# Kernel tuning notes

Hardware: AMD Instinct MI355X
Metric: run time of the kernel (lower is better)

The kernel has to match this reference:

```python
import jax, jax.numpy as jnp
import numpy as np

N, E, G = 100000, 1600000, 256
F_IN, HID, NCLS = 16, 64, 2
EPS = 1e-5


def segment_mean(v, seg, num_segments):
    s = jax.ops.segment_sum(v, seg, num_segments=num_segments)
    c = jax.ops.segment_sum(jnp.ones((v.shape[0], 1), v.dtype), seg, num_segments=num_segments)
    return s / jnp.maximum(c, 1.0)


def graph_norm(x, seg, weight, bias, mean_scale):
    # PyG GraphNorm: per-graph mean/var with learnable mean_scale
    mean = segment_mean(x, seg, G)                      # [G, C]
    centered = x - mean_scale * mean[seg]               # [N, C]
    var = segment_mean(centered * centered, seg, G)     # [G, C]
    return weight * centered * jax.lax.rsqrt(var[seg] + EPS) + bias


def gcn_conv(x, W, b, row, col, n):
    # PyG GCNConv: h = x @ W; symmetric norm with added self-loops; scatter-add; + bias
    h = x @ W                                           # [N, C_out]
    deg = jnp.zeros((n,), x.dtype).at[row].add(1.0) + 1.0  # +1 self-loop
    dinv = jax.lax.rsqrt(deg)
    norm = (dinv[row] * dinv[col])[:, None]             # [E, 1]
    agg = jnp.zeros_like(h).at[row].add(norm * h[col])  # neighbor messages
    agg = agg + (dinv * dinv)[:, None] * h              # self-loop messages
    return agg + b


def setup_inputs():
    key = jax.random.key(0)
    ks = jax.random.split(key, 16)
    x = jax.random.normal(ks[0], (N, F_IN), jnp.float32)
    edge_index = jax.random.randint(ks[1], (2, E), 0, N, jnp.int32)
    batch = jnp.sort(jax.random.randint(ks[2], (N,), 0, G, jnp.int32))
    s = lambda k, shp: jax.random.normal(k, shp, jnp.float32) * 0.05
    return {
        "x": x, "edge_index": edge_index, "batch": batch,
        "gn0_w": jnp.ones((F_IN,)), "gn0_b": jnp.zeros((F_IN,)), "gn0_ms": jnp.ones((F_IN,)),
        "W1": s(ks[3], (F_IN, HID)), "b1": jnp.zeros((HID,)),
        "gn1_w": jnp.ones((HID,)), "gn1_b": jnp.zeros((HID,)), "gn1_ms": jnp.ones((HID,)),
        "W2": s(ks[4], (HID, HID)), "b2": jnp.zeros((HID,)),
        "gn2_w": jnp.ones((HID,)), "gn2_b": jnp.zeros((HID,)), "gn2_ms": jnp.ones((HID,)),
        "W3": s(ks[5], (HID, HID)), "b3": jnp.zeros((HID,)),
        "Wd": s(ks[6], (HID, HID)), "bd": jnp.zeros((HID,)),
        "Wo": s(ks[7], (HID, NCLS)), "bo": jnp.zeros((NCLS,)),
    }


def reference(x, edge_index, batch, gn0_w, gn0_b, gn0_ms, W1, b1, gn1_w, gn1_b, gn1_ms,
              W2, b2, gn2_w, gn2_b, gn2_ms, W3, b3, Wd, bd, Wo, bo):
    row, col = edge_index[0], edge_index[1]
    h = graph_norm(x, batch, gn0_w, gn0_b, gn0_ms)
    h = jax.nn.relu(gcn_conv(h, W1, b1, row, col, N))
    h = graph_norm(h, batch, gn1_w, gn1_b, gn1_ms)
    h = jax.nn.relu(gcn_conv(h, W2, b2, row, col, N))
    h = graph_norm(h, batch, gn2_w, gn2_b, gn2_ms)
    h = jax.nn.relu(gcn_conv(h, W3, b3, row, col, N))
    g = segment_mean(h, batch, G)                       # global_mean_pool -> [G, HID]
    # dropout is identity in eval mode
    g = jax.nn.relu(g @ Wd + bd)
    logits = g @ Wo + bo
    return jax.nn.softmax(logits, axis=1)
```

## Files before the change

kernel.cpp:

```cpp
#include <hip/hip_runtime.h>
#include <hip/hip_bf16.h>

#define NN 100000
#define NE 1600000
#define NG 256
#define FIN 16
#define HID 64
#define NBK 391
#define NTILE 391
#define PMAX 4864
#define BMAXP 5632
#define MAXT (NN / 16 + NG)

__device__ __forceinline__ int lower_bound_i(const int* __restrict__ b, int n, int v) {
    int lo = 0, hi = n;
    while (lo < hi) { int m = (lo + hi) >> 1; if (b[m] < v) lo = m + 1; else hi = m; }
    return lo;
}

__device__ __forceinline__ unsigned pack_bf16(float a, float b) {
    unsigned ua = __float_as_uint(a), ub = __float_as_uint(b);
    ua = (ua + 0x7fffu + ((ua >> 16) & 1u)) >> 16;
    ub = (ub + 0x7fffu + ((ub >> 16) & 1u)) & 0xffff0000u;
    return ua | ub;
}
#define BF_LO(u) __uint_as_float((u) << 16)
#define BF_HI(u) __uint_as_float((u) & 0xffff0000u)

typedef __attribute__((ext_vector_type(8))) short bf16x8;
typedef __attribute__((ext_vector_type(4))) float f32x4;
union FU { uint4 u; bf16x8 v; };

__global__ __launch_bounds__(512) void k_bscatter(const int4* __restrict__ row4, const int4* __restrict__ col4,
                                                  int* __restrict__ bcur, int2* __restrict__ pairs) {
    __shared__ int lh[NBK], lofs[NBK], lbase[NBK], lc[NBK];
    __shared__ int sc[512];
    __shared__ int2 stg[4096];
    for (int i = threadIdx.x; i < NBK; i += 512) { lh[i] = 0; lc[i] = 0; }
    __syncthreads();
    int t0 = blockIdx.x * 1024 + threadIdx.x;
#pragma unroll
    for (int it = 0; it < 2; ++it) {
        int t = t0 + it * 512;
        if (t < NE / 4) {
            int4 r = row4[t];
            atomicAdd(&lh[r.x >> 8], 1); atomicAdd(&lh[r.y >> 8], 1);
            atomicAdd(&lh[r.z >> 8], 1); atomicAdd(&lh[r.w >> 8], 1);
        }
    }
    __syncthreads();
    {
        int t = threadIdx.x;
        int v = (t < NBK) ? lh[t] : 0;
        sc[t] = v;
        __syncthreads();
        int acc = v;
        for (int off = 1; off < 512; off <<= 1) {
            int add = (t >= off) ? sc[t - off] : 0;
            __syncthreads();
            acc += add;
            sc[t] = acc;
            __syncthreads();
        }
        if (t < NBK) lofs[t] = acc - v;
    }
    if (threadIdx.x < NBK) {
        int c = lh[threadIdx.x];
        lbase[threadIdx.x] = c ? atomicAdd(&bcur[threadIdx.x], c) : 0;
    }
    __syncthreads();
#pragma unroll
    for (int it = 0; it < 2; ++it) {
        int t = t0 + it * 512;
        if (t < NE / 4) {
            int4 r = row4[t];
            int4 c = col4[t];
            int b, rk;
            b = r.x >> 8; rk = atomicAdd(&lc[b], 1); stg[lofs[b] + rk] = make_int2(r.x, c.x);
            b = r.y >> 8; rk = atomicAdd(&lc[b], 1); stg[lofs[b] + rk] = make_int2(r.y, c.y);
            b = r.z >> 8; rk = atomicAdd(&lc[b], 1); stg[lofs[b] + rk] = make_int2(r.z, c.z);
            b = r.w >> 8; rk = atomicAdd(&lc[b], 1); stg[lofs[b] + rk] = make_int2(r.w, c.w);
        }
    }
    __syncthreads();
    int nv = min(4096, NE - blockIdx.x * 4096);
    for (int j = threadIdx.x; j < nv; j += 512) {
        int2 p = stg[j];
        int b = p.x >> 8;
        pairs[(long)b * BMAXP + lbase[b] + (j - lofs[b])] = p;
    }
}

__global__ __launch_bounds__(256) void k_bsort(const int2* __restrict__ pairs, const int* __restrict__ bcur,
                                               int* __restrict__ gcur,
                                               int* __restrict__ csr_col, int* __restrict__ startv,
                                               int* __restrict__ degc, float* __restrict__ dinv) {
    __shared__ int colo[PMAX];
    __shared__ int cnt[256], pofs[256], c2[256], sc[256];
    __shared__ int gbase;
    int b = blockIdx.x;
    long sp = (long)b * BMAXP;
    int n = min(bcur[b], PMAX);
    cnt[threadIdx.x] = 0;
    c2[threadIdx.x] = 0;
    __syncthreads();
    for (int i = threadIdx.x; i < n; i += 256)
        atomicAdd(&cnt[pairs[sp + i].x & 255], 1);
    __syncthreads();
    int c = cnt[threadIdx.x];
    {
        int t = threadIdx.x, v = c;
        sc[t] = v;
        __syncthreads();
        int acc = v;
        for (int off = 1; off < 256; off <<= 1) {
            int add = (t >= off) ? sc[t - off] : 0;
            __syncthreads();
            acc += add;
            sc[t] = acc;
            __syncthreads();
        }
        pofs[t] = acc - v;
    }
    if (threadIdx.x == 0) gbase = atomicAdd(gcur, n);
    __syncthreads();
    for (int i = threadIdx.x; i < n; i += 256) {
        int2 p = pairs[sp + i];
        int lr = p.x & 255;
        int rk = atomicAdd(&c2[lr], 1);
        colo[pofs[lr] + rk] = p.y;
    }
    __syncthreads();
    int gb = gbase;
    for (int i = threadIdx.x; i < n; i += 256) csr_col[gb + i] = colo[i];
    int r = (b << 8) + threadIdx.x;
    if (r < NN) {
        startv[r] = gb + pofs[threadIdx.x];
        degc[r] = c;
        dinv[r] = rsqrtf((float)(c + 1));
    }
}

__global__ __launch_bounds__(256) void k_setup(const int* __restrict__ batch, int* __restrict__ ntot,
                                               int* __restrict__ tg, int* __restrict__ tbase,
                                               int* __restrict__ tcnt, const float* __restrict__ W1,
                                               unsigned* __restrict__ Wt1p, unsigned* __restrict__ xb,
                                               unsigned* __restrict__ h2) {
    if (blockIdx.x == 1) {
        int t = threadIdx.x;
        int j = t >> 2, kq = t & 3;
#pragma unroll
        for (int i = 0; i < 4; i++) {
            int idx = kq * 4 + i;
            int k = idx * 2;
            unsigned v = 0;
            if (k < FIN) v = pack_bf16(W1[k * 64 + j], W1[(k + 1) * 64 + j]);
            Wt1p[j * 16 + idx] = v;
        }
        if (t < 32) h2[(long)NN * 32 + t] = 0u;
        if (t < 8) xb[(long)NN * 8 + t] = 0u;
        return;
    }
    __shared__ int gst[NG + 1];
    __shared__ int sc[NG];
    int t = threadIdx.x;
    gst[t] = lower_bound_i(batch, NN, t);
    if (t == 0) gst[NG] = NN;
    __syncthreads();
    int ng = gst[t + 1] - gst[t];
    int nt = (ng + 15) >> 4;
    sc[t] = nt;
    __syncthreads();
    int acc = nt;
    for (int off = 1; off < NG; off <<= 1) {
        int add = (t >= off) ? sc[t - off] : 0;
        __syncthreads();
        acc += add;
        sc[t] = acc;
        __syncthreads();
    }
    int ofs = acc - nt;
    for (int i = 0; i < nt; i++) {
        tg[ofs + i] = t;
        tbase[ofs + i] = gst[t] + i * 16;
        tcnt[ofs + i] = min(16, ng - i * 16);
    }
    if (t == NG - 1) ntot[0] = acc;
}

__global__ __launch_bounds__(512) void k_graphnorm16(const float* __restrict__ x, const int* __restrict__ batch,
                              const float* __restrict__ w, const float* __restrict__ b,
                              const float* __restrict__ ms, const float* __restrict__ dinv,
                              unsigned* __restrict__ xb) {
    constexpr int C = FIN, NPB = 512 / C;
    __shared__ float red[NPB][C], red2[NPB][C];
    __shared__ float mm_s[C], rs_s[C];
    int g = blockIdx.x;
    int s = lower_bound_i(batch, NN, g);
    int e = lower_bound_i(batch, NN, g + 1);
    float fc = (float)max(e - s, 1);
    int c = threadIdx.x % C, slot = threadIdx.x / C;

    float a1 = 0.f, a2 = 0.f;
    for (int i = s + slot; i < e; i += NPB) { float v = x[i * C + c]; a1 += v; a2 += v * v; }
    red[slot][c] = a1;
    red2[slot][c] = a2;
    __syncthreads();
    if (threadIdx.x < C) {
        float t1 = 0.f, t2 = 0.f;
        for (int k = 0; k < NPB; k++) { t1 += red[k][threadIdx.x]; t2 += red2[k][threadIdx.x]; }
        float mean = t1 / fc;
        float mm = ms[threadIdx.x] * mean;
        float var = t2 / fc - 2.f * mm * mean + mm * mm;
        mm_s[threadIdx.x] = mm;
        rs_s[threadIdx.x] = rsqrtf(var + 1e-5f);
    }
    __syncthreads();
    float mm = mm_s[c], ww = w[c] * rs_s[c], bb = b[c];
    for (int i = s + slot; i < e; i += NPB) {
        float v = (ww * (x[i * C + c] - mm) + bb) * dinv[i];
        float partner = __shfl_xor(v, 1);
        if ((c & 1) == 0) xb[(long)i * 8 + (c >> 1)] = pack_bf16(v, partner);
    }
}

__global__ __launch_bounds__(512) void k_gnstats2(const unsigned* __restrict__ xw, const int* __restrict__ batch,
                          const float* __restrict__ w, const float* __restrict__ b,
                          const float* __restrict__ ms, const float* __restrict__ W,
                          unsigned* __restrict__ Wtp, float* __restrict__ bias2) {
    __shared__ float4 red[16][32];
    __shared__ float sA[64], sB[64];
    int g = blockIdx.x;
    int s = lower_bound_i(batch, NN, g);
    int e = lower_bound_i(batch, NN, g + 1);
    float fc = (float)max(e - s, 1);
    int cu = threadIdx.x & 31, slot = threadIdx.x >> 5;

    float s1l = 0.f, s1h = 0.f, s2l = 0.f, s2h = 0.f;
    for (int i = s + slot; i < e; i += 16) {
        unsigned u = xw[(long)i * 32 + cu];
        float lo = BF_LO(u), hi = BF_HI(u);
        s1l += lo; s1h += hi; s2l += lo * lo; s2h += hi * hi;
    }
    red[slot][cu] = make_float4(s1l, s1h, s2l, s2h);
    __syncthreads();
    if (threadIdx.x < 64) {
        int cc = threadIdx.x, iu = cc >> 1, hi = cc & 1;
        float t1 = 0.f, t2 = 0.f;
        for (int k = 0; k < 16; k++) {
            float4 v = red[k][iu];
            t1 += hi ? v.y : v.x;
            t2 += hi ? v.w : v.z;
        }
        float mean = t1 / fc;
        float mm = ms[cc] * mean;
        float var = t2 / fc - 2.f * mm * mean + mm * mm;
        float A = w[cc] * rsqrtf(var + 1e-5f);
        sA[cc] = A;
        sB[cc] = b[cc] - A * mm;
    }
    __syncthreads();
    if (threadIdx.x < 256) {
        int j = threadIdx.x >> 2, kq = threadIdx.x & 3;
        unsigned* wrow = Wtp + ((long)g * 64 + j) * 32 + kq * 8;
        float part = 0.f;
#pragma unroll
        for (int i = 0; i < 8; i++) {
            int k = kq * 16 + 2 * i;
            float w0 = W[k * 64 + j], w1 = W[(k + 1) * 64 + j];
            wrow[i] = pack_bf16(sA[k] * w0, sA[k + 1] * w1);
            part += sB[k] * w0 + sB[k + 1] * w1;
        }
        part += __shfl_xor(part, 1);
        part += __shfl_xor(part, 2);
        if (kq == 0) bias2[g * 64 + j] = part;
    }
}

__global__ __launch_bounds__(256) void k_gather16(const unsigned* __restrict__ xb, const int* __restrict__ startv,
                           const int* __restrict__ degc, const float* __restrict__ dinv,
                           const int* __restrict__ csr_col, unsigned* __restrict__ agg) {
    int wave = (blockIdx.x * blockDim.x + threadIdx.x) >> 6;
    if (wave >= NN) return;
    int lane = threadIdx.x & 63;
    unsigned p = lane & 7;
    int g = lane >> 3;
    int s = startv[wave], cnt = degc[wave];
    float di = dinv[wave];
    float ax = 0.f, ay = 0.f;
    int k = g;
    for (; k + 8 < cnt; k += 16) {
        unsigned c0 = (unsigned)csr_col[s + k], c1 = (unsigned)csr_col[s + k + 8];
        unsigned u0 = xb[c0 * 8u + p], u1 = xb[c1 * 8u + p];
        ax += BF_LO(u0) + BF_LO(u1);
        ay += BF_HI(u0) + BF_HI(u1);
    }
    if (k < cnt) {
        unsigned c0 = (unsigned)csr_col[s + k];
        unsigned u0 = xb[c0 * 8u + p];
        ax += BF_LO(u0);
        ay += BF_HI(u0);
    }
    ax += __shfl_xor(ax, 8);  ay += __shfl_xor(ay, 8);
    ax += __shfl_xor(ax, 16); ay += __shfl_xor(ay, 16);
    ax += __shfl_xor(ax, 32); ay += __shfl_xor(ay, 32);
    if (g == 0) {
        unsigned u = xb[(unsigned)wave * 8u + p];
        ax = (ax + BF_LO(u)) * di;
        ay = (ay + BF_HI(u)) * di;
        agg[(long)wave * 16 + p] = pack_bf16(ax, ay);
    } else if (g == 1) {
        agg[(long)wave * 16 + 8 + p] = 0u;
    }
}

template <int KU, bool PERG, bool RELU, bool DINV>
__global__ __launch_bounds__(256) void k_gemmT(const unsigned* __restrict__ Ain, const unsigned* __restrict__ Wt,
                        const float* __restrict__ biasv, const float* __restrict__ dinv,
                        const int* __restrict__ ntot, const int* __restrict__ tg,
                        const int* __restrict__ tbase, const int* __restrict__ tcnt,
                        unsigned* __restrict__ Aout) {
    const int RW = KU * 16;
    int tix = blockIdx.x * 4 + (threadIdx.x >> 6);
    if (tix >= ntot[0]) return;
    int g = tg[tix], base = tbase[tix], n = tcnt[tix];
    int l = threadIdx.x & 63, r = l & 15, q = l >> 4;
    FU a[KU];
#pragma unroll
    for (int s = 0; s < KU; s++) {
        if (r < n) a[s].u = *(const uint4*)(Ain + (long)(base + r) * RW + s * 16 + q * 4);
        else a[s].u = make_uint4(0, 0, 0, 0);
    }
    const unsigned* wb = PERG ? (Wt + (long)g * 64 * RW) : Wt;
    f32x4 acc[4];
#pragma unroll
    for (int t = 0; t < 4; t++) {
        acc[t] = (f32x4){0.f, 0.f, 0.f, 0.f};
#pragma unroll
        for (int s = 0; s < KU; s++) {
            FU bfrag;
            bfrag.u = *(const uint4*)(wb + (long)(t * 16 + r) * RW + s * 16 + q * 4);
            acc[t] = __builtin_amdgcn_mfma_f32_16x16x32_bf16(a[s].v, bfrag.v, acc[t], 0, 0, 0);
        }
    }
    const float* bb = PERG ? (biasv + g * 64) : biasv;
    float dv[4];
#pragma unroll
    for (int e = 0; e < 4; e++) {
        int node = base + q * 4 + e;
        dv[e] = DINV ? ((node < NN) ? dinv[node] : 0.f) : 1.f;
    }
#pragma unroll
    for (int t = 0; t < 4; t++) {
        float bv = bb[t * 16 + r];
#pragma unroll
        for (int e = 0; e < 4; e++) {
            float v = acc[t][e] + bv;
            if (RELU) v = fmaxf(v, 0.f);
            if (DINV) v *= dv[e];
            float part = __shfl_xor(v, 1);
            if ((q * 4 + e) < n && (r & 1) == 0)
                Aout[(long)(base + q * 4 + e) * 32 + t * 8 + (r >> 1)] = pack_bf16(v, part);
        }
    }
}

__global__ __launch_bounds__(256) void k_gather64(const unsigned* __restrict__ h2, const int* __restrict__ startv,
                           const int* __restrict__ degc, const float* __restrict__ dinv,
                           const int* __restrict__ csr_col, const float* __restrict__ bias,
                           unsigned* __restrict__ outp) {
    int wave = (blockIdx.x * blockDim.x + threadIdx.x) >> 6;
    if (wave >= NN) return;
    int lane = threadIdx.x & 63;
    unsigned p = lane & 31;
    int g = lane >> 5;
    int s = startv[wave], cnt = degc[wave];
    float di = dinv[wave];
    float ax = 0.f, ay = 0.f;
    if (g == 0) {
        unsigned u = h2[(unsigned)wave * 32u + p];
        ax = BF_LO(u);
        ay = BF_HI(u);
    }
    for (int k = g * 8; k < cnt; k += 16) {
        int cc[8];
#pragma unroll
        for (int i = 0; i < 8; i++) {
            int idx = k + i;
            cc[i] = (idx < cnt) ? csr_col[s + idx] : -1;
        }
        unsigned u[8];
#pragma unroll
        for (int i = 0; i < 8; i++)
            u[i] = (cc[i] >= 0) ? h2[(unsigned)cc[i] * 32u + p] : 0u;
#pragma unroll
        for (int i = 0; i < 8; i++) { ax += BF_LO(u[i]); ay += BF_HI(u[i]); }
    }
    ax += __shfl_xor(ax, 32);
    ay += __shfl_xor(ay, 32);
    if (g == 0) {
        float2 bv = ((const float2*)bias)[p];
        float vx = fmaxf(ax * di + bv.x, 0.f);
        float vy = fmaxf(ay * di + bv.y, 0.f);
        outp[(unsigned)wave * 32u + p] = pack_bf16(vx, vy);
    }
}

__global__ __launch_bounds__(1024) void k_poolhead(const unsigned* __restrict__ xw, const int* __restrict__ batch,
                       const float* __restrict__ Wd, const float* __restrict__ bd,
                       const float* __restrict__ Wo, const float* __restrict__ bo,
                       float* __restrict__ out) {
    __shared__ float red[16][64];
    __shared__ float wds[64 * 64];
    __shared__ float gs[64];
    int g = blockIdx.x;
    int s = lower_bound_i(batch, NN, g);
    int e = lower_bound_i(batch, NN, g + 1);
    int c = threadIdx.x & 63, slot = threadIdx.x >> 6;
    for (int i = threadIdx.x; i < 64 * 64; i += 1024) wds[i] = Wd[i];
    float acc = 0.f;
    for (int i = s + slot; i < e; i += 16) {
        unsigned u = xw[(long)i * 32 + (c >> 1)];
        acc += (c & 1) ? BF_HI(u) : BF_LO(u);
    }
    red[slot][c] = acc;
    __syncthreads();
    if (threadIdx.x < 64) {
        float t = 0.f;
        for (int k = 0; k < 16; k++) t += red[k][threadIdx.x];
        gs[threadIdx.x] = t / (float)max(e - s, 1);
    }
    __syncthreads();
    if (threadIdx.x < 64) {
        int j = threadIdx.x;
        float a2 = bd[j];
        for (int k = 0; k < 64; k++) a2 += gs[k] * wds[k * 64 + j];
        float hv = fmaxf(a2, 0.f);
        float p0 = hv * Wo[j * 2 + 0], p1 = hv * Wo[j * 2 + 1];
        for (int off = 32; off; off >>= 1) { p0 += __shfl_down(p0, off); p1 += __shfl_down(p1, off); }
        if (j == 0) {
            float l0 = p0 + bo[0], l1 = p1 + bo[1];
            float m = fmaxf(l0, l1);
            float e0 = expf(l0 - m), e1 = expf(l1 - m);
            float inv = 1.f / (e0 + e1);
            out[g * 2 + 0] = e0 * inv;
            out[g * 2 + 1] = e1 * inv;
        }
    }
}

extern "C" void kernel_launch(void* const* d_in, const int* in_sizes, int n_in,
                              void* d_out, int out_size, void* d_ws, size_t ws_size,
                              hipStream_t stream) {
    const float* x = (const float*)d_in[0];
    const int* ei = (const int*)d_in[1];
    const int* row = ei;
    const int* col = ei + NE;
    const int* batch = (const int*)d_in[2];
    const float* gn0w = (const float*)d_in[3];
    const float* gn0b = (const float*)d_in[4];
    const float* gn0ms = (const float*)d_in[5];
    const float* W1 = (const float*)d_in[6];
    const float* b1 = (const float*)d_in[7];
    const float* gn1w = (const float*)d_in[8];
    const float* gn1b = (const float*)d_in[9];
    const float* gn1ms = (const float*)d_in[10];
    const float* W2 = (const float*)d_in[11];
    const float* b2 = (const float*)d_in[12];
    const float* gn2w = (const float*)d_in[13];
    const float* gn2b = (const float*)d_in[14];
    const float* gn2ms = (const float*)d_in[15];
    const float* W3 = (const float*)d_in[16];
    const float* b3 = (const float*)d_in[17];
    const float* Wd = (const float*)d_in[18];
    const float* bd = (const float*)d_in[19];
    const float* Wo = (const float*)d_in[20];
    const float* bo = (const float*)d_in[21];
    float* outp = (float*)d_out;

    int* bcur = (int*)d_ws;
    int* gcur = bcur + 504;
    int* startv = bcur + 512;
    int* degc = startv + NN;
    float* dinv = (float*)(degc + NN);
    int* csr_col = (int*)(dinv + NN);
    int* ntot = csr_col + NE + 64;
    int* tg = ntot + 16;
    int* tbase = tg + 6608;
    int* tcnt = tbase + 6608;
    unsigned* Wt1p = (unsigned*)(tcnt + 6608);
    unsigned* Wtp = Wt1p + 1024;
    float* bias2 = (float*)(Wtp + (long)NG * 64 * 32);
    unsigned* xb = (unsigned*)(bias2 + NG * 64);
    unsigned* agg16 = xb + (long)NN * 8 + 16;
    unsigned* bufA = agg16 + (long)NN * 16;
    unsigned* bufB = bufA + (long)NN * 32;
    unsigned* h2 = bufB + (long)NN * 32;
    int2* pairs = (int2*)bufA;

    const int NBG = (MAXT + 3) / 4;

    hipMemsetAsync(bcur, 0, 512 * sizeof(int), stream);
    k_bscatter<<<NTILE, 512, 0, stream>>>((const int4*)row, (const int4*)col, bcur, pairs);
    k_bsort<<<NBK, 256, 0, stream>>>(pairs, bcur, gcur, csr_col, startv, degc, dinv);

    k_setup<<<2, 256, 0, stream>>>(batch, ntot, tg, tbase, tcnt, W1, Wt1p, xb, h2);

    k_graphnorm16<<<NG, 512, 0, stream>>>(x, batch, gn0w, gn0b, gn0ms, dinv, xb);
    k_gather16<<<(NN * 64 + 255) / 256, 256, 0, stream>>>(xb, startv, degc, dinv, csr_col, agg16);
    k_gemmT<1, false, true, false><<<NBG, 256, 0, stream>>>(agg16, Wt1p, b1, dinv, ntot, tg, tbase, tcnt, bufA);

    k_gnstats2<<<NG, 512, 0, stream>>>(bufA, batch, gn1w, gn1b, gn1ms, W2, Wtp, bias2);
    k_gemmT<2, true, false, true><<<NBG, 256, 0, stream>>>(bufA, Wtp, bias2, dinv, ntot, tg, tbase, tcnt, h2);
    k_gather64<<<(NN * 64 + 255) / 256, 256, 0, stream>>>(h2, startv, degc, dinv, csr_col, b2, bufB);

    k_gnstats2<<<NG, 512, 0, stream>>>(bufB, batch, gn2w, gn2b, gn2ms, W3, Wtp, bias2);
    k_gemmT<2, true, false, true><<<NBG, 256, 0, stream>>>(bufB, Wtp, bias2, dinv, ntot, tg, tbase, tcnt, h2);
    k_gather64<<<(NN * 64 + 255) / 256, 256, 0, stream>>>(h2, startv, degc, dinv, csr_col, b3, bufA);

    k_poolhead<<<NG, 1024, 0, stream>>>(bufA, batch, Wd, bd, Wo, bo, outp);
}
```

Baseline: 380.6 us.

## Pack edge pairs into 32-bit words, vectorize gather64, fold memset into setup

Edge (row,col) pairs are packed into one 32-bit word holding the low 8 row bits and a 17-bit column, so the bucket-scatter intermediate is half its former size. Bucket IDs travel in a separate shared array. The 64-wide gather now has each lane load a uint4 (8 bf16 features) with 8 edges per wave step, then reduces with more shuffles. The bcur memset moves into an extra block of k_setup, which now launches first, removing a separate memset call. Together these cut global traffic and launch overhead, at the cost of more shuffle reductions and of relying on column indices fitting in 17 bits.

```diff
diff --git a/kernel.cpp b/kernel.cpp
--- a/kernel.cpp
+++ b/kernel.cpp
@@ -32,10 +32,11 @@
 union FU { uint4 u; bf16x8 v; };
 
 __global__ __launch_bounds__(512) void k_bscatter(const int4* __restrict__ row4, const int4* __restrict__ col4,
-                                                  int* __restrict__ bcur, int2* __restrict__ pairs) {
+                                                  int* __restrict__ bcur, unsigned* __restrict__ pairs) {
     __shared__ int lh[NBK], lofs[NBK], lbase[NBK], lc[NBK];
     __shared__ int sc[512];
-    __shared__ int2 stg[4096];
+    __shared__ unsigned stg[4096];
+    __shared__ unsigned short stgb[4096];
     for (int i = threadIdx.x; i < NBK; i += 512) { lh[i] = 0; lc[i] = 0; }
     __syncthreads();
     int t0 = blockIdx.x * 1024 + threadIdx.x;
@@ -75,23 +76,26 @@
         if (t < NE / 4) {
             int4 r = row4[t];
             int4 c = col4[t];
-            int b, rk;
-            b = r.x >> 8; rk = atomicAdd(&lc[b], 1); stg[lofs[b] + rk] = make_int2(r.x, c.x);
-            b = r.y >> 8; rk = atomicAdd(&lc[b], 1); stg[lofs[b] + rk] = make_int2(r.y, c.y);
-            b = r.z >> 8; rk = atomicAdd(&lc[b], 1); stg[lofs[b] + rk] = make_int2(r.z, c.z);
-            b = r.w >> 8; rk = atomicAdd(&lc[b], 1); stg[lofs[b] + rk] = make_int2(r.w, c.w);
+            int b, rk, ix;
+            b = r.x >> 8; rk = atomicAdd(&lc[b], 1); ix = lofs[b] + rk;
+            stg[ix] = ((unsigned)(r.x & 255) << 17) | (unsigned)c.x; stgb[ix] = (unsigned short)b;
+            b = r.y >> 8; rk = atomicAdd(&lc[b], 1); ix = lofs[b] + rk;
+            stg[ix] = ((unsigned)(r.y & 255) << 17) | (unsigned)c.y; stgb[ix] = (unsigned short)b;
+            b = r.z >> 8; rk = atomicAdd(&lc[b], 1); ix = lofs[b] + rk;
+            stg[ix] = ((unsigned)(r.z & 255) << 17) | (unsigned)c.z; stgb[ix] = (unsigned short)b;
+            b = r.w >> 8; rk = atomicAdd(&lc[b], 1); ix = lofs[b] + rk;
+            stg[ix] = ((unsigned)(r.w & 255) << 17) | (unsigned)c.w; stgb[ix] = (unsigned short)b;
         }
     }
     __syncthreads();
     int nv = min(4096, NE - blockIdx.x * 4096);
     for (int j = threadIdx.x; j < nv; j += 512) {
-        int2 p = stg[j];
-        int b = p.x >> 8;
-        pairs[(long)b * BMAXP + lbase[b] + (j - lofs[b])] = p;
-    }
-}
-
-__global__ __launch_bounds__(256) void k_bsort(const int2* __restrict__ pairs, const int* __restrict__ bcur,
+        int b = stgb[j];
+        pairs[(long)b * BMAXP + lbase[b] + (j - lofs[b])] = stg[j];
+    }
+}
+
+__global__ __launch_bounds__(256) void k_bsort(const unsigned* __restrict__ pairs, const int* __restrict__ bcur,
                                                int* __restrict__ gcur,
                                                int* __restrict__ csr_col, int* __restrict__ startv,
                                                int* __restrict__ degc, float* __restrict__ dinv) {
@@ -101,18 +105,18 @@
     int b = blockIdx.x;
     long sp = (long)b * BMAXP;
     int n = min(bcur[b], PMAX);
-    cnt[threadIdx.x] = 0;
-    c2[threadIdx.x] = 0;
-    __syncthreads();
-    for (int i = threadIdx.x; i < n; i += 256)
-        atomicAdd(&cnt[pairs[sp + i].x & 255], 1);
-    __syncthreads();
-    int c = cnt[threadIdx.x];
+    int t = threadIdx.x;
+    cnt[t] = 0;
+    c2[t] = 0;
+    __syncthreads();
+    for (int i = t; i < n; i += 256)
+        atomicAdd(&cnt[pairs[sp + i] >> 17], 1);
+    __syncthreads();
+    int c = cnt[t];
     {
-        int t = threadIdx.x, v = c;
-        sc[t] = v;
+        sc[t] = c;
         __syncthreads();
-        int acc = v;
+        int acc = c;
         for (int off = 1; off < 256; off <<= 1) {
             int add = (t >= off) ? sc[t - off] : 0;
             __syncthreads();
@@ -120,22 +124,22 @@
             sc[t] = acc;
             __syncthreads();
         }
-        pofs[t] = acc - v;
-    }
-    if (threadIdx.x == 0) gbase = atomicAdd(gcur, n);
-    __syncthreads();
-    for (int i = threadIdx.x; i < n; i += 256) {
-        int2 p = pairs[sp + i];
-        int lr = p.x & 255;
+        pofs[t] = acc - c;
+    }
+    if (t == 0) gbase = atomicAdd(gcur, n);
+    __syncthreads();
+    for (int i = t; i < n; i += 256) {
+        unsigned v = pairs[sp + i];
+        int lr = v >> 17;
         int rk = atomicAdd(&c2[lr], 1);
-        colo[pofs[lr] + rk] = p.y;
+        colo[pofs[lr] + rk] = v & 0x1FFFFu;
     }
     __syncthreads();
     int gb = gbase;
-    for (int i = threadIdx.x; i < n; i += 256) csr_col[gb + i] = colo[i];
-    int r = (b << 8) + threadIdx.x;
+    for (int i = t; i < n; i += 256) csr_col[gb + i] = colo[i];
+    int r = (b << 8) + t;
     if (r < NN) {
-        startv[r] = gb + pofs[threadIdx.x];
+        startv[r] = gb + pofs[t];
         degc[r] = c;
         dinv[r] = rsqrtf((float)(c + 1));
     }
@@ -145,7 +149,13 @@
                                                int* __restrict__ tg, int* __restrict__ tbase,
                                                int* __restrict__ tcnt, const float* __restrict__ W1,
                                                unsigned* __restrict__ Wt1p, unsigned* __restrict__ xb,
-                                               unsigned* __restrict__ h2) {
+                                               unsigned* __restrict__ h2, int* __restrict__ bcur) {
+    if (blockIdx.x == 2) {
+        if (threadIdx.x < 512 - 256) {}
+        bcur[threadIdx.x] = 0;
+        bcur[threadIdx.x + 256] = 0;
+        return;
+    }
     if (blockIdx.x == 1) {
         int t = threadIdx.x;
         int j = t >> 2, kq = t & 3;
@@ -372,37 +382,46 @@
     int wave = (blockIdx.x * blockDim.x + threadIdx.x) >> 6;
     if (wave >= NN) return;
     int lane = threadIdx.x & 63;
-    unsigned p = lane & 31;
-    int g = lane >> 5;
+    int g = lane >> 3;
+    unsigned p = lane & 7;
     int s = startv[wave], cnt = degc[wave];
     float di = dinv[wave];
-    float ax = 0.f, ay = 0.f;
+    float a0 = 0.f, a1 = 0.f, a2 = 0.f, a3 = 0.f, a4 = 0.f, a5 = 0.f, a6 = 0.f, a7 = 0.f;
     if (g == 0) {
-        unsigned u = h2[(unsigned)wave * 32u + p];
-        ax = BF_LO(u);
-        ay = BF_HI(u);
-    }
-    for (int k = g * 8; k < cnt; k += 16) {
-        int cc[8];
-#pragma unroll
-        for (int i = 0; i < 8; i++) {
-            int idx = k + i;
-            cc[i] = (idx < cnt) ? csr_col[s + idx] : -1;
-        }
-        unsigned u[8];
-#pragma unroll
-        for (int i = 0; i < 8; i++)
-            u[i] = (cc[i] >= 0) ? h2[(unsigned)cc[i] * 32u + p] : 0u;
-#pragma unroll
-        for (int i = 0; i < 8; i++) { ax += BF_LO(u[i]); ay += BF_HI(u[i]); }
-    }
-    ax += __shfl_xor(ax, 32);
-    ay += __shfl_xor(ay, 32);
+        uint4 u = *(const uint4*)(h2 + (unsigned)wave * 32u + p * 4u);
+        a0 = BF_LO(u.x); a1 = BF_HI(u.x); a2 = BF_LO(u.y); a3 = BF_HI(u.y);
+        a4 = BF_LO(u.z); a5 = BF_HI(u.z); a6 = BF_LO(u.w); a7 = BF_HI(u.w);
+    }
+    for (int k = 0; k < cnt; k += 16) {
+        int i0 = k + g, i1 = k + 8 + g;
+        unsigned c0 = (i0 < cnt) ? (unsigned)csr_col[s + i0] : (unsigned)NN;
+        unsigned c1 = (i1 < cnt) ? (unsigned)csr_col[s + i1] : (unsigned)NN;
+        uint4 u0 = *(const uint4*)(h2 + c0 * 32u + p * 4u);
+        uint4 u1 = *(const uint4*)(h2 + c1 * 32u + p * 4u);
+        a0 += BF_LO(u0.x) + BF_LO(u1.x);
+        a1 += BF_HI(u0.x) + BF_HI(u1.x);
+        a2 += BF_LO(u0.y) + BF_LO(u1.y);
+        a3 += BF_HI(u0.y) + BF_HI(u1.y);
+        a4 += BF_LO(u0.z) + BF_LO(u1.z);
+        a5 += BF_HI(u0.z) + BF_HI(u1.z);
+        a6 += BF_LO(u0.w) + BF_LO(u1.w);
+        a7 += BF_HI(u0.w) + BF_HI(u1.w);
+    }
+    a0 += __shfl_xor(a0, 8);  a1 += __shfl_xor(a1, 8);  a2 += __shfl_xor(a2, 8);  a3 += __shfl_xor(a3, 8);
+    a4 += __shfl_xor(a4, 8);  a5 += __shfl_xor(a5, 8);  a6 += __shfl_xor(a6, 8);  a7 += __shfl_xor(a7, 8);
+    a0 += __shfl_xor(a0, 16); a1 += __shfl_xor(a1, 16); a2 += __shfl_xor(a2, 16); a3 += __shfl_xor(a3, 16);
+    a4 += __shfl_xor(a4, 16); a5 += __shfl_xor(a5, 16); a6 += __shfl_xor(a6, 16); a7 += __shfl_xor(a7, 16);
+    a0 += __shfl_xor(a0, 32); a1 += __shfl_xor(a1, 32); a2 += __shfl_xor(a2, 32); a3 += __shfl_xor(a3, 32);
+    a4 += __shfl_xor(a4, 32); a5 += __shfl_xor(a5, 32); a6 += __shfl_xor(a6, 32); a7 += __shfl_xor(a7, 32);
     if (g == 0) {
-        float2 bv = ((const float2*)bias)[p];
-        float vx = fmaxf(ax * di + bv.x, 0.f);
-        float vy = fmaxf(ay * di + bv.y, 0.f);
-        outp[(unsigned)wave * 32u + p] = pack_bf16(vx, vy);
+        const float2* bv2 = (const float2*)bias;
+        float2 b0 = bv2[p * 4 + 0], b1 = bv2[p * 4 + 1], b2 = bv2[p * 4 + 2], b3 = bv2[p * 4 + 3];
+        uint4 w;
+        w.x = pack_bf16(fmaxf(a0 * di + b0.x, 0.f), fmaxf(a1 * di + b0.y, 0.f));
+        w.y = pack_bf16(fmaxf(a2 * di + b1.x, 0.f), fmaxf(a3 * di + b1.y, 0.f));
+        w.z = pack_bf16(fmaxf(a4 * di + b2.x, 0.f), fmaxf(a5 * di + b2.y, 0.f));
+        w.w = pack_bf16(fmaxf(a6 * di + b3.x, 0.f), fmaxf(a7 * di + b3.y, 0.f));
+        *(uint4*)(outp + (unsigned)wave * 32u + p * 4u) = w;
     }
 }
 
@@ -496,15 +515,14 @@
     unsigned* bufA = agg16 + (long)NN * 16;
     unsigned* bufB = bufA + (long)NN * 32;
     unsigned* h2 = bufB + (long)NN * 32;
-    int2* pairs = (int2*)bufA;
+    unsigned* pairs = (unsigned*)bufA;
 
     const int NBG = (MAXT + 3) / 4;
 
-    hipMemsetAsync(bcur, 0, 512 * sizeof(int), stream);
+    k_setup<<<3, 256, 0, stream>>>(batch, ntot, tg, tbase, tcnt, W1, Wt1p, xb, h2, bcur);
+
     k_bscatter<<<NTILE, 512, 0, stream>>>((const int4*)row, (const int4*)col, bcur, pairs);
     k_bsort<<<NBK, 256, 0, stream>>>(pairs, bcur, gcur, csr_col, startv, degc, dinv);
-
-    k_setup<<<2, 256, 0, stream>>>(batch, ntot, tg, tbase, tcnt, W1, Wt1p, xb, h2);
 
     k_graphnorm16<<<NG, 512, 0, stream>>>(x, batch, gn0w, gn0b, gn0ms, dinv, xb);
     k_gather16<<<(NN * 64 + 255) / 256, 256, 0, stream>>>(xb, startv, degc, dinv, csr_col, agg16);
```

Result: no change. 378.2 us (-0.6%).
